# Kernel tuning notes

Measured on AMD Instinct MI355X. Metric: run time of the kernel, lower is better.

Reference implementation:

```python
import jax, jax.numpy as jnp
import numpy as np

V, H, L = 32000, 512, 1
B, S = 16, 64


def setup_inputs() -> dict:
    key = jax.random.key(0)
    ks = jax.random.split(key, 10)
    inp = {
        "target_seqs": jax.random.randint(ks[0], (B, S), 0, V),
        "thought": jax.random.normal(ks[1], (1, B, H), dtype=jnp.float32),
        "hidden": jax.random.normal(ks[2], (L, B, H), dtype=jnp.float32),
        # parameters
        "emb": jax.random.normal(ks[3], (V, H), dtype=jnp.float32) * 0.02,
        "W_ih": jax.random.normal(ks[4], (3 * H, 2 * H), dtype=jnp.float32) * (1.0 / np.sqrt(H)),
        "W_hh": jax.random.normal(ks[5], (3 * H, H), dtype=jnp.float32) * (1.0 / np.sqrt(H)),
        "b_ih": jax.random.normal(ks[6], (3 * H,), dtype=jnp.float32) * 0.01,
        "b_hh": jax.random.normal(ks[7], (3 * H,), dtype=jnp.float32) * 0.01,
        "W_out": jax.random.normal(ks[8], (V, H), dtype=jnp.float32) * (1.0 / np.sqrt(H)),
        "b_out": jax.random.normal(ks[9], (V,), dtype=jnp.float32) * 0.01,
    }
    return inp


def gru_layer(x_sbd, h0, W_ih, W_hh, b_ih, b_hh):
    # x_sbd: [S,B,2H]; h0: [B,H]. Torch GRU cell math.
    # Precompute input projections for all timesteps: [S,B,3H]
    gi = jnp.einsum('sbd,gd->sbg', x_sbd, W_ih) + b_ih

    def step(h, gi_t):
        gh = h @ W_hh.T + b_hh                       # [B,3H]
        i_r, i_z, i_n = jnp.split(gi_t, 3, axis=-1)
        h_r, h_z, h_n = jnp.split(gh, 3, axis=-1)
        r = jax.nn.sigmoid(i_r + h_r)
        z = jax.nn.sigmoid(i_z + h_z)
        n = jnp.tanh(i_n + r * h_n)
        h_new = (1.0 - z) * n + z * h
        return h_new, h_new

    h_last, ys = jax.lax.scan(step, h0, gi)
    return ys, h_last                                 # [S,B,H], [B,H]


def reference(target_seqs, thought, hidden, emb, W_ih, W_hh, b_ih, b_hh, W_out, b_out):
    embedded = emb[target_seqs]                        # [B,S,H]
    # fused broadcast-concat replacing the python double loop
    th = jnp.broadcast_to(thought[0][:, None, :], embedded.shape)  # [B,S,H]
    rnn_input = jnp.concatenate([embedded, th], axis=-1)           # [B,S,2H]
    x_sbd = jnp.transpose(rnn_input, (1, 0, 2))                    # [S,B,2H]
    ys, h_last = gru_layer(x_sbd, hidden[0], W_ih, W_hh, b_ih, b_hh)
    output = jnp.transpose(ys, (1, 0, 2))              # [B,S,H]
    logits = jnp.einsum('bsh,vh->bsv', output, W_out) + b_out
    logp = jax.nn.log_softmax(logits, axis=-1)         # [B,S,V]
    return logp, h_last[None]                          # hidden: [1,B,H]
```

## Files before the change

kernel.cpp:

```cpp
#include <hip/hip_runtime.h>

typedef unsigned int u32;
typedef unsigned short u16;
typedef short s16x8 __attribute__((ext_vector_type(8)));
typedef float f32x4 __attribute__((ext_vector_type(4)));

#define SENT 0xFFFFFFFFu

__device__ __forceinline__ u16 f2bf(float f) {
  u32 u = __float_as_uint(f);
  u32 r = (u + 0x7fffu + ((u >> 16) & 1u)) >> 16;
  return (u16)r;
}

__device__ __forceinline__ uint4 load_u4_bypass(const u32* p) {
  uint4 r;
  asm volatile("global_load_dwordx4 %0, %1, off sc0 sc1\n\ts_waitcnt vmcnt(0)"
               : "=v"(r) : "v"(p) : "memory");
  return r;
}

__device__ __forceinline__ void gload16(const u16* g, u16* l) {
  __builtin_amdgcn_global_load_lds(
      (const __attribute__((address_space(1))) unsigned int*)(g),
      (__attribute__((address_space(3))) unsigned int*)(l), 16, 0, 0);
}

__global__ __launch_bounds__(256) void pre_kernel(const float* __restrict__ W_ih,
                                                  u16* __restrict__ wih_bf,
                                                  const int* __restrict__ tseq,
                                                  const float* __restrict__ emb,
                                                  const float* __restrict__ thought,
                                                  u16* __restrict__ x,
                                                  u32* __restrict__ hbase) {
  int blk = blockIdx.x, tid = threadIdx.x;
  if (blk < 1536) {
    int i = blk * 256 + tid;
    float4 v = reinterpret_cast<const float4*>(W_ih)[i];
    u32 lo = (u32)f2bf(v.x) | ((u32)f2bf(v.y) << 16);
    u32 hi = (u32)f2bf(v.z) | ((u32)f2bf(v.w) << 16);
    reinterpret_cast<uint2*>(wih_bf)[i] = make_uint2(lo, hi);
  } else if (blk < 2560) {
    int m = blk - 1536;
    int s = m >> 4, b = m & 15;
    int k = tid * 4;
    const float* src = (k < 512) ? emb + (size_t)tseq[b * 64 + s] * 512 + k
                                 : thought + b * 512 + (k - 512);
    float4 v = *reinterpret_cast<const float4*>(src);
    *reinterpret_cast<uint2*>(x + (size_t)m * 1024 + k) =
        make_uint2((u32)f2bf(v.x) | ((u32)f2bf(v.y) << 16),
                   (u32)f2bf(v.z) | ((u32)f2bf(v.w) << 16));
  } else {
    int i = (blk - 2560) * 256 + tid;
    reinterpret_cast<uint4*>(hbase)[i] = make_uint4(SENT, SENT, SENT, SENT);
  }
}

template <bool LSE>
__global__ __launch_bounds__(256) void gemm_bt_kernel(const u16* __restrict__ A,
                                                      const u16* __restrict__ Bm,
                                                      const float* __restrict__ bias,
                                                      float* __restrict__ C,
                                                      int M_, int N_, int K_,
                                                      float* __restrict__ partials, int nnb) {
  __shared__ u16 sA[2][4096];
  __shared__ u16 sB[2][4096];
  __shared__ float pm[2][128];
  __shared__ float ps[2][128];
  int bid = blockIdx.x;
  int nwg8 = gridDim.x >> 3;
  int wgid = (bid & 7) * nwg8 + (bid >> 3);
  int mb = wgid & 7, nb = wgid >> 3;
  int m0 = mb * 128, n0 = nb * 128;
  int tid = threadIdx.x;
  int wave = tid >> 6, lane = tid & 63;
  int wm = wave >> 1, wn = wave & 1;
  int l16 = lane & 15, quad = lane >> 4;
  int c0 = wave * 128 + lane, c1 = c0 + 64;
  int r0 = c0 >> 2, co0 = (c0 & 3) * 8;
  int r1 = c1 >> 2, co1 = (c1 & 3) * 8;
  const u16* gA0 = A + (size_t)(m0 + r0) * K_ + co0;
  const u16* gA1 = A + (size_t)(m0 + r1) * K_ + co1;
  const u16* gB0 = Bm + (size_t)(n0 + r0) * K_ + co0;
  const u16* gB1 = Bm + (size_t)(n0 + r1) * K_ + co1;
  int wbase = wave * 1024;

  auto STAGE = [&](int buf, int k0) {
    gload16(gA0 + k0, &sA[buf][wbase]);
    gload16(gA1 + k0, &sA[buf][wbase + 512]);
    gload16(gB0 + k0, &sB[buf][wbase]);
    gload16(gB1 + k0, &sB[buf][wbase + 512]);
  };

  f32x4 acc[4][4];
  for (int i = 0; i < 4; ++i)
    for (int j = 0; j < 4; ++j) acc[i][j] = (f32x4){0.f, 0.f, 0.f, 0.f};

  int NK = K_ >> 5;
  STAGE(0, 0);
  __syncthreads();
  int cur = 0;
  for (int ks = 0; ks < NK; ++ks) {
    if (ks + 1 < NK) STAGE(cur ^ 1, (ks + 1) * 32);
    s16x8 af[4], bfr[4];
    for (int mt = 0; mt < 4; ++mt)
      af[mt] = *reinterpret_cast<const s16x8*>(&sA[cur][(wm * 64 + mt * 16 + l16) * 32 + quad * 8]);
    for (int nt = 0; nt < 4; ++nt)
      bfr[nt] = *reinterpret_cast<const s16x8*>(&sB[cur][(wn * 64 + nt * 16 + l16) * 32 + quad * 8]);
    for (int mt = 0; mt < 4; ++mt)
      for (int nt = 0; nt < 4; ++nt)
        acc[mt][nt] = __builtin_amdgcn_mfma_f32_16x16x32_bf16(af[mt], bfr[nt], acc[mt][nt], 0, 0, 0);
    if (ks + 1 < NK) {
      __syncthreads();
      cur ^= 1;
    }
  }

  int rbase = wm * 64 + quad * 4;
  int cbase = n0 + wn * 64 + l16;
  for (int nt = 0; nt < 4; ++nt) {
    float bv = bias[cbase + nt * 16];
    for (int mt = 0; mt < 4; ++mt)
      for (int r = 0; r < 4; ++r) acc[mt][nt][r] += bv;
  }
  for (int mt = 0; mt < 4; ++mt)
    for (int r = 0; r < 4; ++r) {
      int row = m0 + rbase + mt * 16 + r;
      for (int nt = 0; nt < 4; ++nt)
        C[(size_t)row * N_ + cbase + nt * 16] = acc[mt][nt][r];
    }
  if (LSE) {
    for (int mt = 0; mt < 4; ++mt)
      for (int r = 0; r < 4; ++r) {
        float mx = acc[mt][0][r];
        for (int nt = 1; nt < 4; ++nt) mx = fmaxf(mx, acc[mt][nt][r]);
        for (int d = 1; d < 16; d <<= 1) mx = fmaxf(mx, __shfl_xor(mx, d));
        float sm = 0.f;
        for (int nt = 0; nt < 4; ++nt) sm += __expf(acc[mt][nt][r] - mx);
        for (int d = 1; d < 16; d <<= 1) sm += __shfl_xor(sm, d);
        if (l16 == 0) {
          int rr = wm * 64 + mt * 16 + quad * 4 + r;
          pm[wn][rr] = mx;
          ps[wn][rr] = sm;
        }
      }
    __syncthreads();
    if (tid < 128) {
      float m1 = pm[0][tid], m2 = pm[1][tid];
      float s1 = ps[0][tid], s2 = ps[1][tid];
      float Mx = fmaxf(m1, m2);
      float Sx = s1 * __expf(m1 - Mx) + s2 * __expf(m2 - Mx);
      float* p = partials + ((size_t)(m0 + tid) * nnb + nb) * 2;
      p[0] = Mx;
      p[1] = Sx;
    }
  }
}

__global__ __launch_bounds__(256, 2) void gru_kernel(const float* __restrict__ gi,
                                                     const float* __restrict__ W_hh,
                                                     const float* __restrict__ b_hh,
                                                     const float* __restrict__ hidden,
                                                     u32* __restrict__ hbase,
                                                     u16* __restrict__ ys,
                                                     float* __restrict__ hlast,
                                                     const float* __restrict__ wout_f32,
                                                     u16* __restrict__ wout_bf) {
  __shared__ u16 sW[48 * 520];
  __shared__ float h_s[576];
  int wg = blockIdx.x;
  int tid = threadIdx.x;

  if (wg >= 512) {
    for (int i = (wg - 512) * 256 + tid; i < 4096000; i += 256 * 256) {
      float4 v = reinterpret_cast<const float4*>(wout_f32)[i];
      u32 lo = (u32)f2bf(v.x) | ((u32)f2bf(v.y) << 16);
      u32 hi = (u32)f2bf(v.z) | ((u32)f2bf(v.w) << 16);
      reinterpret_cast<uint2*>(wout_bf)[i] = make_uint2(lo, hi);
    }
    return;
  }

  int b = wg >> 5, g = wg & 31;
  for (int e = tid * 4; e < 48 * 512; e += 1024) {
    int lr = e >> 9, col = e & 511;
    int grow = (lr >> 4) * 512 + g * 16 + (lr & 15);
    float4 v = *reinterpret_cast<const float4*>(W_hh + (size_t)grow * 512 + col);
    u32 lo = (u32)f2bf(v.x) | ((u32)f2bf(v.y) << 16);
    u32 hi = (u32)f2bf(v.z) | ((u32)f2bf(v.w) << 16);
    *reinterpret_cast<uint2*>(&sW[lr * 520 + col]) = make_uint2(lo, hi);
  }
  int grp = tid >> 4, l16 = tid & 15;
  int j = g * 16 + grp;
  float bhr = 0.f, bhz = 0.f, bhn = 0.f;
  if (l16 == 0) { bhr = b_hh[j]; bhz = b_hh[512 + j]; bhn = b_hh[1024 + j]; }
  int j0 = tid * 4;
  if (tid < 128) {
    float4 f = *reinterpret_cast<const float4*>(hidden + b * 512 + j0);
    *reinterpret_cast<float4*>(&h_s[j0 + ((j0 >> 5) << 2)]) = f;
  }
  __syncthreads();

  for (int t = 0; t < 64; ++t) {
    float gir = 0.f, giz = 0.f, gin = 0.f;
    if (l16 == 0) {
      size_t gib = ((size_t)t * 16 + b) * 1536;
      gir = gi[gib + j]; giz = gi[gib + 512 + j]; gin = gi[gib + 1024 + j];
    }
    if (t > 0) {
      const u32* hp = hbase + (size_t)(t - 1) * 8192 + b * 512;
      if (tid < 32) {
        const u32* fp = hp + tid * 16;
        u32 v = __hip_atomic_load(fp, __ATOMIC_RELAXED, __HIP_MEMORY_SCOPE_AGENT);
        while (v == SENT) {
          __builtin_amdgcn_s_sleep(2);
          v = __hip_atomic_load(fp, __ATOMIC_RELAXED, __HIP_MEMORY_SCOPE_AGENT);
        }
      }
      __syncthreads();
      if (tid < 128) {
        uint4 v = load_u4_bypass(hp + j0);
        while (v.x == SENT || v.y == SENT || v.z == SENT || v.w == SENT) {
          __builtin_amdgcn_s_sleep(1);
          v = load_u4_bypass(hp + j0);
        }
        float4 f;
        f.x = __uint_as_float(v.x); f.y = __uint_as_float(v.y);
        f.z = __uint_as_float(v.z); f.w = __uint_as_float(v.w);
        *reinterpret_cast<float4*>(&h_s[j0 + ((j0 >> 5) << 2)]) = f;
      }
      __syncthreads();
    }
    float hreg[32];
    int hb2 = l16 * 36;
    for (int c4 = 0; c4 < 4; ++c4) {
      float4 x0 = *reinterpret_cast<const float4*>(&h_s[hb2 + c4 * 8]);
      float4 x1 = *reinterpret_cast<const float4*>(&h_s[hb2 + c4 * 8 + 4]);
      hreg[c4 * 8 + 0] = x0.x; hreg[c4 * 8 + 1] = x0.y;
      hreg[c4 * 8 + 2] = x0.z; hreg[c4 * 8 + 3] = x0.w;
      hreg[c4 * 8 + 4] = x1.x; hreg[c4 * 8 + 5] = x1.y;
      hreg[c4 * 8 + 6] = x1.z; hreg[c4 * 8 + 7] = x1.w;
    }
    float a0 = 0.f, a1 = 0.f, a2 = 0.f;
    const u16* wr0 = &sW[grp * 520 + l16 * 32];
    const u16* wr1 = wr0 + 16 * 520;
    const u16* wr2 = wr0 + 32 * 520;
    for (int c4 = 0; c4 < 4; ++c4) {
      uint4 w0 = *reinterpret_cast<const uint4*>(wr0 + c4 * 8);
      uint4 w1 = *reinterpret_cast<const uint4*>(wr1 + c4 * 8);
      uint4 w2 = *reinterpret_cast<const uint4*>(wr2 + c4 * 8);
      const float* hh = &hreg[c4 * 8];
      a0 += __uint_as_float(w0.x << 16) * hh[0] + __uint_as_float(w0.x & 0xffff0000u) * hh[1];
      a0 += __uint_as_float(w0.y << 16) * hh[2] + __uint_as_float(w0.y & 0xffff0000u) * hh[3];
      a0 += __uint_as_float(w0.z << 16) * hh[4] + __uint_as_float(w0.z & 0xffff0000u) * hh[5];
      a0 += __uint_as_float(w0.w << 16) * hh[6] + __uint_as_float(w0.w & 0xffff0000u) * hh[7];
      a1 += __uint_as_float(w1.x << 16) * hh[0] + __uint_as_float(w1.x & 0xffff0000u) * hh[1];
      a1 += __uint_as_float(w1.y << 16) * hh[2] + __uint_as_float(w1.y & 0xffff0000u) * hh[3];
      a1 += __uint_as_float(w1.z << 16) * hh[4] + __uint_as_float(w1.z & 0xffff0000u) * hh[5];
      a1 += __uint_as_float(w1.w << 16) * hh[6] + __uint_as_float(w1.w & 0xffff0000u) * hh[7];
      a2 += __uint_as_float(w2.x << 16) * hh[0] + __uint_as_float(w2.x & 0xffff0000u) * hh[1];
      a2 += __uint_as_float(w2.y << 16) * hh[2] + __uint_as_float(w2.y & 0xffff0000u) * hh[3];
      a2 += __uint_as_float(w2.z << 16) * hh[4] + __uint_as_float(w2.z & 0xffff0000u) * hh[5];
      a2 += __uint_as_float(w2.w << 16) * hh[6] + __uint_as_float(w2.w & 0xffff0000u) * hh[7];
    }
    for (int d = 1; d < 16; d <<= 1) {
      a0 += __shfl_xor(a0, d);
      a1 += __shfl_xor(a1, d);
      a2 += __shfl_xor(a2, d);
    }
    if (l16 == 0) {
      float er = __expf(-(gir + a0 + bhr));
      float ez = __expf(-(giz + a1 + bhz));
      float r = __fdividef(1.f, 1.f + er);
      float z = __fdividef(1.f, 1.f + ez);
      float xn = gin + r * (a2 + bhn);
      float en = __expf(2.f * xn);
      float n = 1.f - __fdividef(2.f, en + 1.f);
      float hprev = h_s[j + ((j >> 5) << 2)];
      float hv = (1.f - z) * n + z * hprev;
      __hip_atomic_store(hbase + (size_t)t * 8192 + b * 512 + j, __float_as_uint(hv),
                         __ATOMIC_RELAXED, __HIP_MEMORY_SCOPE_AGENT);
      ys[((size_t)b * 64 + t) * 512 + j] = f2bf(hv);
      if (t == 63) hlast[b * 512 + j] = hv;
    }
  }
}

__global__ __launch_bounds__(256) void lse_sub_kernel(const float* __restrict__ partials,
                                                      float* __restrict__ out, int nnb) {
  __shared__ float sM[4], sS[4];
  int row = blockIdx.x;
  int tid = threadIdx.x;
  int lane = tid & 63, wv = tid >> 6;
  float M = -INFINITY, S = 0.f;
  if (tid < nnb) {
    const float* p = partials + ((size_t)row * nnb + tid) * 2;
    M = p[0]; S = p[1];
  }
  for (int d = 1; d < 64; d <<= 1) {
    float m2 = __shfl_xor(M, d), s2 = __shfl_xor(S, d);
    if (m2 > M) { float tt = M; M = m2; m2 = tt; tt = S; S = s2; s2 = tt; }
    if (s2 > 0.f) S += s2 * __expf(m2 - M);
  }
  if (lane == 0) { sM[wv] = M; sS[wv] = S; }
  __syncthreads();
  M = sM[0]; S = sS[0];
  for (int w = 1; w < 4; ++w) {
    float m2 = sM[w], s2 = sS[w];
    if (m2 > M) { float tt = M; M = m2; m2 = tt; tt = S; S = s2; s2 = tt; }
    if (s2 > 0.f) S += s2 * __expf(m2 - M);
  }
  float l = M + logf(S);
  float4* po = reinterpret_cast<float4*>(out + (size_t)row * 32000);
  for (int i = tid; i < 8000; i += 256) {
    float4 v = po[i];
    v.x -= l; v.y -= l; v.z -= l; v.w -= l;
    po[i] = v;
  }
}

extern "C" void kernel_launch(void* const* d_in, const int* in_sizes, int n_in,
                              void* d_out, int out_size, void* d_ws, size_t ws_size,
                              hipStream_t stream) {
  const int* tseq = (const int*)d_in[0];
  const float* thought = (const float*)d_in[1];
  const float* hidden = (const float*)d_in[2];
  const float* emb = (const float*)d_in[3];
  const float* W_ih = (const float*)d_in[4];
  const float* W_hh = (const float*)d_in[5];
  const float* b_ih = (const float*)d_in[6];
  const float* b_hh = (const float*)d_in[7];
  const float* W_out = (const float*)d_in[8];
  const float* b_out = (const float*)d_in[9];
  float* out = (float*)d_out;

  char* ws = (char*)d_ws;
  size_t off = 0;
  auto alloc = [&](size_t bytes) {
    void* p = ws + off;
    off = (off + bytes + 255) & ~(size_t)255;
    return p;
  };
  u16* wout_bf = (u16*)alloc((size_t)32000 * 512 * 2);
  u16* wih_bf  = (u16*)alloc((size_t)1536 * 1024 * 2);
  u16* x_bf    = (u16*)alloc((size_t)1024 * 1024 * 2);
  u16* ys_bf   = (u16*)alloc((size_t)1024 * 512 * 2);
  float* gi    = (float*)alloc((size_t)1024 * 1536 * 4);
  u32* hbase   = (u32*)alloc((size_t)64 * 16 * 512 * 4);
  float* partials = (float*)alloc((size_t)1024 * 250 * 2 * 4);
  (void)ws_size; (void)in_sizes; (void)n_in; (void)out_size;

  pre_kernel<<<3072, 256, 0, stream>>>(W_ih, wih_bf, tseq, emb, thought, x_bf, hbase);
  gemm_bt_kernel<false><<<96, 256, 0, stream>>>(x_bf, wih_bf, b_ih, gi,
                                                1024, 1536, 1024, nullptr, 0);
  gru_kernel<<<768, 256, 0, stream>>>(gi, W_hh, b_hh, hidden, hbase, ys_bf,
                                      out + 32768000, W_out, wout_bf);
  gemm_bt_kernel<true><<<2000, 256, 0, stream>>>(ys_bf, wout_bf, b_out, out,
                                                 1024, 32000, 512, partials, 250);
  lse_sub_kernel<<<1024, 256, 0, stream>>>(partials, out, 250);
}
```

Measured before the change: 460.9 us.

## Use 128x256 tiles for output projection GEMM with fused partial log-sum-exp

Adds a separate output-projection GEMM kernel that uses 128x256 tiles, with each of the four waves covering a 128x64 slice, in place of 128x128 tiles. The aim is to reuse each A tile across twice as many columns, cut the grid in half and halve the number of log-sum-exp partials written and later read by the subtract kernel. In exchange each wave holds twice as many accumulators, which adds register pressure and may lower occupancy. The input-projection GEMM keeps the old 128x128 tiling, now without the template parameter.

```diff
diff --git a/kernel.cpp b/kernel.cpp
--- a/kernel.cpp
+++ b/kernel.cpp
@@ -56,17 +56,13 @@
   }
 }
 
-template <bool LSE>
 __global__ __launch_bounds__(256) void gemm_bt_kernel(const u16* __restrict__ A,
                                                       const u16* __restrict__ Bm,
                                                       const float* __restrict__ bias,
                                                       float* __restrict__ C,
-                                                      int M_, int N_, int K_,
-                                                      float* __restrict__ partials, int nnb) {
+                                                      int M_, int N_, int K_) {
   __shared__ u16 sA[2][4096];
   __shared__ u16 sB[2][4096];
-  __shared__ float pm[2][128];
-  __shared__ float ps[2][128];
   int bid = blockIdx.x;
   int nwg8 = gridDim.x >> 3;
   int wgid = (bid & 7) * nwg8 + (bid >> 3);
@@ -129,31 +125,106 @@
       for (int nt = 0; nt < 4; ++nt)
         C[(size_t)row * N_ + cbase + nt * 16] = acc[mt][nt][r];
     }
-  if (LSE) {
-    for (int mt = 0; mt < 4; ++mt)
-      for (int r = 0; r < 4; ++r) {
-        float mx = acc[mt][0][r];
-        for (int nt = 1; nt < 4; ++nt) mx = fmaxf(mx, acc[mt][nt][r]);
-        for (int d = 1; d < 16; d <<= 1) mx = fmaxf(mx, __shfl_xor(mx, d));
-        float sm = 0.f;
-        for (int nt = 0; nt < 4; ++nt) sm += __expf(acc[mt][nt][r] - mx);
-        for (int d = 1; d < 16; d <<= 1) sm += __shfl_xor(sm, d);
-        if (l16 == 0) {
-          int rr = wm * 64 + mt * 16 + quad * 4 + r;
-          pm[wn][rr] = mx;
-          ps[wn][rr] = sm;
-        }
+}
+
+__global__ __launch_bounds__(256, 2) void gemm_bt256_kernel(const u16* __restrict__ A,
+                                                            const u16* __restrict__ Bm,
+                                                            const float* __restrict__ bias,
+                                                            float* __restrict__ C,
+                                                            int M_, int N_, int K_,
+                                                            float* __restrict__ partials, int nnb) {
+  __shared__ u16 sA[2][4096];
+  __shared__ u16 sB[2][8192];
+  __shared__ float pm[4][128];
+  __shared__ float ps[4][128];
+  int bid = blockIdx.x;
+  int nwg8 = gridDim.x >> 3;
+  int wgid = (bid & 7) * nwg8 + (bid >> 3);
+  int mb = wgid & 7, nb = wgid >> 3;
+  int m0 = mb * 128, n0 = nb * 256;
+  int tid = threadIdx.x;
+  int wave = tid >> 6, lane = tid & 63;
+  int wn = wave;
+  int l16 = lane & 15, quad = lane >> 4;
+  int ca0 = wave * 64 + lane;
+  int ca1 = 256 + wave * 64 + lane;
+  const u16* gA0 = A + (size_t)(m0 + (ca0 >> 2)) * K_ + (ca0 & 3) * 8;
+  const u16* gA1 = A + (size_t)(m0 + (ca1 >> 2)) * K_ + (ca1 & 3) * 8;
+  const u16* gBp[4];
+  for (int i = 0; i < 4; ++i) {
+    int bc = i * 256 + wave * 64 + lane;
+    gBp[i] = Bm + (size_t)(n0 + (bc >> 2)) * K_ + (bc & 3) * 8;
+  }
+  int wb8 = wave * 64 * 8;
+
+  auto STAGE = [&](int buf, int k0) {
+    gload16(gA0 + k0, &sA[buf][wb8]);
+    gload16(gA1 + k0, &sA[buf][2048 + wb8]);
+    for (int i = 0; i < 4; ++i)
+      gload16(gBp[i] + k0, &sB[buf][i * 2048 + wb8]);
+  };
+
+  f32x4 acc[8][4];
+  for (int i = 0; i < 8; ++i)
+    for (int j = 0; j < 4; ++j) acc[i][j] = (f32x4){0.f, 0.f, 0.f, 0.f};
+
+  int NK = K_ >> 5;
+  STAGE(0, 0);
+  __syncthreads();
+  int cur = 0;
+  for (int ks = 0; ks < NK; ++ks) {
+    if (ks + 1 < NK) STAGE(cur ^ 1, (ks + 1) * 32);
+    s16x8 af[8], bfr[4];
+    for (int mt = 0; mt < 8; ++mt)
+      af[mt] = *reinterpret_cast<const s16x8*>(&sA[cur][(mt * 16 + l16) * 32 + quad * 8]);
+    for (int nt = 0; nt < 4; ++nt)
+      bfr[nt] = *reinterpret_cast<const s16x8*>(&sB[cur][(wn * 64 + nt * 16 + l16) * 32 + quad * 8]);
+    for (int mt = 0; mt < 8; ++mt)
+      for (int nt = 0; nt < 4; ++nt)
+        acc[mt][nt] = __builtin_amdgcn_mfma_f32_16x16x32_bf16(af[mt], bfr[nt], acc[mt][nt], 0, 0, 0);
+    if (ks + 1 < NK) {
+      __syncthreads();
+      cur ^= 1;
+    }
+  }
+
+  int cbase = n0 + wn * 64 + l16;
+  for (int nt = 0; nt < 4; ++nt) {
+    float bv = bias[cbase + nt * 16];
+    for (int mt = 0; mt < 8; ++mt)
+      for (int r = 0; r < 4; ++r) acc[mt][nt][r] += bv;
+  }
+  for (int mt = 0; mt < 8; ++mt)
+    for (int r = 0; r < 4; ++r) {
+      int row = m0 + mt * 16 + quad * 4 + r;
+      for (int nt = 0; nt < 4; ++nt)
+        C[(size_t)row * N_ + cbase + nt * 16] = acc[mt][nt][r];
+    }
+  for (int mt = 0; mt < 8; ++mt)
+    for (int r = 0; r < 4; ++r) {
+      float mx = acc[mt][0][r];
+      for (int nt = 1; nt < 4; ++nt) mx = fmaxf(mx, acc[mt][nt][r]);
+      for (int d = 1; d < 16; d <<= 1) mx = fmaxf(mx, __shfl_xor(mx, d));
+      float sm = 0.f;
+      for (int nt = 0; nt < 4; ++nt) sm += __expf(acc[mt][nt][r] - mx);
+      for (int d = 1; d < 16; d <<= 1) sm += __shfl_xor(sm, d);
+      if (l16 == 0) {
+        int rr = mt * 16 + quad * 4 + r;
+        pm[wn][rr] = mx;
+        ps[wn][rr] = sm;
       }
-    __syncthreads();
-    if (tid < 128) {
-      float m1 = pm[0][tid], m2 = pm[1][tid];
-      float s1 = ps[0][tid], s2 = ps[1][tid];
-      float Mx = fmaxf(m1, m2);
-      float Sx = s1 * __expf(m1 - Mx) + s2 * __expf(m2 - Mx);
-      float* p = partials + ((size_t)(m0 + tid) * nnb + nb) * 2;
-      p[0] = Mx;
-      p[1] = Sx;
-    }
+    }
+  __syncthreads();
+  if (tid < 128) {
+    float M = pm[0][tid], S = ps[0][tid];
+    for (int w = 1; w < 4; ++w) {
+      float m2 = pm[w][tid], s2 = ps[w][tid];
+      if (m2 > M) { float tt = M; M = m2; m2 = tt; tt = S; S = s2; s2 = tt; }
+      if (s2 > 0.f) S += s2 * __expf(m2 - M);
+    }
+    float* p = partials + ((size_t)(m0 + tid) * nnb + nb) * 2;
+    p[0] = M;
+    p[1] = S;
   }
 }
 
@@ -347,15 +418,14 @@
   u16* ys_bf   = (u16*)alloc((size_t)1024 * 512 * 2);
   float* gi    = (float*)alloc((size_t)1024 * 1536 * 4);
   u32* hbase   = (u32*)alloc((size_t)64 * 16 * 512 * 4);
-  float* partials = (float*)alloc((size_t)1024 * 250 * 2 * 4);
+  float* partials = (float*)alloc((size_t)1024 * 125 * 2 * 4);
   (void)ws_size; (void)in_sizes; (void)n_in; (void)out_size;
 
   pre_kernel<<<3072, 256, 0, stream>>>(W_ih, wih_bf, tseq, emb, thought, x_bf, hbase);
-  gemm_bt_kernel<false><<<96, 256, 0, stream>>>(x_bf, wih_bf, b_ih, gi,
-                                                1024, 1536, 1024, nullptr, 0);
+  gemm_bt_kernel<<<96, 256, 0, stream>>>(x_bf, wih_bf, b_ih, gi, 1024, 1536, 1024);
   gru_kernel<<<768, 256, 0, stream>>>(gi, W_hh, b_hh, hidden, hbase, ys_bf,
                                       out + 32768000, W_out, wout_bf);
-  gemm_bt_kernel<true><<<2000, 256, 0, stream>>>(ys_bf, wout_bf, b_out, out,
-                                                 1024, 32000, 512, partials, 250);
-  lse_sub_kernel<<<1024, 256, 0, stream>>>(partials, out, 250);
-}
+  gemm_bt256_kernel<<<1000, 256, 0, stream>>>(ys_bf, wout_bf, b_out, out,
+                                              1024, 32000, 512, partials, 125);
+  lse_sub_kernel<<<1024, 256, 0, stream>>>(partials, out, 125);
+}
```

Result: no change. 467.4 us (+1.4%).
